# Kernel optimization log

Hardware: AMD Instinct MI355X
Metric: run time of the kernel (lower is better)

Reference implementation:

```python
import jax, jax.numpy as jnp
import numpy as np

B, T, DIN, DOUT = 64, 128, 32, 64
HE, HD, K = 512, 1024, 12
NPH, NPL = 512, 64
# per-sample decoder parameter layout: Whh, bh, Wih, C, D
_PSI_SHAPES = [(HD, HD), (HD,), (DIN, HD), (HD, DOUT), (DIN, DOUT - DIN)]
_PSI_SIZES = [int(np.prod(s)) for s in _PSI_SHAPES]
_PSI_OFF = np.cumsum([0] + _PSI_SIZES)
NPSI = int(_PSI_OFF[-1])


def _xavier(key, shape):
    fan_in, fan_out = shape[-2], shape[-1]
    lim = np.sqrt(6.0 / (fan_in + fan_out))
    return jax.random.uniform(key, shape, jnp.float32, -lim, lim)


def setup_inputs() -> dict:
    key = jax.random.key(0)
    ks = jax.random.split(key, 16)
    gru_bias = jnp.concatenate([jnp.zeros(HD), jnp.ones(HD)])  # z-gate bias init to 1
    return {
        'inputs': jax.random.normal(ks[0], (B, T, DIN), jnp.float32),
        'outputs': jax.random.normal(ks[1], (B, T, DOUT), jnp.float32),
        'eps': jax.random.normal(ks[2], (B, K), jnp.float32),
        'state': jnp.zeros((B, HD), jnp.float32),
        'enc_Wih': _xavier(ks[3], (3 * HE, DOUT)),
        'enc_Whh': _xavier(ks[4], (3 * HE, HE)),
        'enc_bih': jnp.zeros(3 * HE, jnp.float32),
        'enc_bhh': jnp.zeros(3 * HE, jnp.float32),
        'to_mu': _xavier(ks[5], (HE, K)),
        'to_lsigma': _xavier(ks[6], (HE, K)),
        'to_lsigma_bias': -0.5 * jnp.ones(K, jnp.float32),
        'psi_W1': _xavier(ks[7], (K, NPH)),
        'psi_b1': jnp.zeros(NPH, jnp.float32),
        'psi_W2': _xavier(ks[8], (NPH, NPL)),
        'psi_b2': jnp.zeros(NPL, jnp.float32),
        'psi_W3': _xavier(ks[9], (NPL, NPSI)) * 0.05,
        'psi_b3': jnp.zeros(NPSI, jnp.float32),
        'gru_Wih': _xavier(ks[10], (DIN, 2 * HD)),
        'gru_Whh': _xavier(ks[11], (HD, 2 * HD)),
        'gru_bias': gru_bias,
    }


def _forward(inputs, outputs, eps, state, enc_Wih, enc_Whh, enc_bih, enc_bhh,
             to_mu, to_lsigma, to_lsigma_bias, psi_W1, psi_b1, psi_W2, psi_b2,
             psi_W3, psi_b3, gru_Wih, gru_Whh, gru_bias):
    # ---- encoder: shared GRUCell over time (torch GRUCell semantics) ----
    def enc_step(h, x):
        gi = x @ enc_Wih.T + enc_bih          # [B,3HE]
        gh = h @ enc_Whh.T + enc_bhh
        ir, iz, inn = jnp.split(gi, 3, axis=-1)
        hr, hz, hn = jnp.split(gh, 3, axis=-1)
        r = jax.nn.sigmoid(ir + hr)
        z = jax.nn.sigmoid(iz + hz)
        n = jnp.tanh(inn + r * hn)
        return (1.0 - z) * n + z * h, None
    h0 = jnp.zeros((outputs.shape[0], HE), outputs.dtype)
    h_enc, _ = jax.lax.scan(enc_step, h0, jnp.swapaxes(outputs, 0, 1))

    mu = h_enc @ to_mu
    logstd = h_enc @ to_lsigma + to_lsigma_bias
    z_lat = mu + eps * jnp.exp(logstd)

    # ---- hypernetwork: decode per-sample GRU params ----
    psi = (jnp.tanh(z_lat @ psi_W1 + psi_b1) @ psi_W2 + psi_b2) @ psi_W3 + psi_b3  # [B,NPSI]
    parts = [psi[:, _PSI_OFF[i]:_PSI_OFF[i + 1]].reshape((-1,) + _PSI_SHAPES[i])
             for i in range(5)]
    Whh_b, bh_b, Wih_b, C_b, D_b = parts

    # ---- per-sample partial GRU over time (batched via einsum) ----
    def dec_step(h, x):
        gx = x @ gru_Wih                       # [B,2HD] shared gates
        gh = h @ gru_Whh
        r = jax.nn.sigmoid(gx[:, :HD] + gh[:, :HD] + gru_bias[:HD])
        zt = jax.nn.sigmoid(gx[:, HD:] + gh[:, HD:] + gru_bias[HD:])
        eta = jnp.tanh(jnp.einsum('bi,bih->bh', x, Wih_b)
                       + r * jnp.einsum('bh,bhg->bg', h, Whh_b) + bh_b)
        h_new = zt * h + (1.0 - zt) * eta
        return h_new, h_new
    _, dec = jax.lax.scan(dec_step, state, jnp.swapaxes(inputs, 0, 1))
    dec = jnp.swapaxes(dec, 0, 1)              # [B,T,HD]

    # residual_output with HUMAN_SIZE > input_dim: concat(raw inputs, inputs@D)
    resid = jnp.concatenate([inputs, jnp.einsum('bti,bio->bto', inputs, D_b)], axis=-1)
    yhats = jnp.einsum('bth,bho->bto', dec, C_b) + resid
    states = jax.lax.stop_gradient(dec[:, -1, :])
    return yhats, mu, logstd, states


def reference(inputs, outputs, eps, state, enc_Wih, enc_Whh, enc_bih, enc_bhh,
              to_mu, to_lsigma, to_lsigma_bias, psi_W1, psi_b1, psi_W2, psi_b2,
              psi_W3, psi_b3, gru_Wih, gru_Whh, gru_bias):
    return _forward(inputs, outputs, eps, state, enc_Wih, enc_Whh, enc_bih, enc_bhh,
                    to_mu, to_lsigma, to_lsigma_bias, psi_W1, psi_b1, psi_W2, psi_b2,
                    psi_W3, psi_b3, gru_Wih, gru_Whh, gru_bias)
```

## Files before the change

kernel.cpp:

```cpp
#include <hip/hip_runtime.h>
#include <stdint.h>

#define B_ 64
#define T_ 128
#define DIN_ 32
#define DOUT_ 64
#define HE_ 512
#define HD_ 1024
#define NPSI_ 1148928
#define PPS_ 100352

typedef short bf16x8 __attribute__((ext_vector_type(8)));
typedef float f32x4 __attribute__((ext_vector_type(4)));
typedef int   i32x4 __attribute__((ext_vector_type(4)));

__device__ __forceinline__ unsigned short f2b(float f){
  unsigned u = __float_as_uint(f);
  u += 0x7fffu + ((u>>16)&1u);
  return (unsigned short)(u>>16);
}
__device__ __forceinline__ float b2f(unsigned short s){
  return __uint_as_float(((unsigned)s)<<16);
}
__device__ __forceinline__ float sigm_(float x){
  float e = __expf(-x);
  return 1.f/(1.f+e);
}
__device__ __forceinline__ float tanh_(float x){
  float e = __expf(2.f*x);
  return 1.f - 2.f/(e+1.f);
}
__device__ __forceinline__ void glds16(const void* g, void* l) {
  __builtin_amdgcn_global_load_lds(
      (const __attribute__((address_space(1))) unsigned int*)g,
      (__attribute__((address_space(3))) unsigned int*)l, 16, 0, 0);
}

__global__ __launch_bounds__(512) void k_prep(
    const float* __restrict__ enc_Whh, const float* __restrict__ enc_Wih,
    const float* __restrict__ gru_Whh, const float* __restrict__ state,
    unsigned short* __restrict__ encW_f, unsigned short* __restrict__ encI_f,
    signed char* __restrict__ gru_q, float* __restrict__ scales_g,
    unsigned short* __restrict__ h_dec)
{
  __shared__ unsigned gmax_s;
  __shared__ __align__(16) signed char gq[512];
  int blk = blockIdx.x, tid = threadIdx.x;
  if (blk < 1536) {
    int nt = blk >> 4, kt = blk & 15;
    int c = tid >> 5, k = tid & 31;
    float v = enc_Whh[(size_t)(nt*16 + c)*HE_ + kt*32 + k];
    int l = c + ((k>>3)<<4), jj = k & 7;
    encW_f[(size_t)(nt*16 + kt)*512 + l*8 + jj] = f2b(v);
  } else if (blk < 1728) {
    int f = blk - 1536; int nt = f >> 1, kt = f & 1;
    int c = tid >> 5, k = tid & 31;
    float v = enc_Wih[(size_t)(nt*16 + c)*DOUT_ + kt*32 + k];
    int l = c + ((k>>3)<<4), jj = k & 7;
    encI_f[(size_t)(nt*2 + kt)*512 + l*8 + jj] = f2b(v);
  } else if (blk < 5824) {
    int f = blk - 1728; int nt = f >> 5, kt = f & 31;
    int k = tid >> 4, c = tid & 15;
    float v = gru_Whh[(size_t)(kt*32 + k)*2048 + nt*16 + c];
    int l = c + ((k>>3)<<4), jj = k & 7;
    if (tid == 0) gmax_s = 0;
    __syncthreads();
    float av = fabsf(v);
    #pragma unroll
    for (int d = 1; d < 64; d <<= 1) av = fmaxf(av, __shfl_xor(av, d));
    if ((tid & 63) == 0) atomicMax(&gmax_s, __float_as_uint(av));
    __syncthreads();
    float m = __uint_as_float(gmax_s);
    float inv = (m > 0.f) ? (127.f/m) : 0.f;
    gq[l*8 + jj] = (signed char)(int)rintf(v*inv);
    __syncthreads();
    if (tid < 32)
      *(i32x4*)(gru_q + (size_t)(nt*32 + kt)*512 + tid*16) = *(const i32x4*)(&gq[tid*16]);
    if (tid == 0) scales_g[nt*32 + kt] = m;
  } else {
    int b = blk - 5824;
    h_dec[(size_t)b*HD_ + tid]       = f2b(state[(size_t)b*HD_ + tid]);
    h_dec[(size_t)b*HD_ + 512 + tid] = f2b(state[(size_t)b*HD_ + 512 + tid]);
  }
}

__global__ __launch_bounds__(128) void k_encoder(
    const float* __restrict__ outputs, const float* __restrict__ bih, const float* __restrict__ bhh,
    const unsigned short* __restrict__ encW_f, const unsigned short* __restrict__ encI_f,
    unsigned short* __restrict__ h_buf, float* __restrict__ h_enc, unsigned int* __restrict__ bar)
{
  __shared__ __align__(16) unsigned short h_bf[16*520];
  __shared__ __align__(16) unsigned short xa[16*72];
  __shared__ float part[64*16];
  int tid = threadIdx.x, wv = tid >> 6, lane = tid & 63;
  int g = blockIdx.x >> 5, bg = blockIdx.x & 31;
  int c0 = bg*16, gs = g*8;
  for (int i = tid; i < 16*520; i += 128) h_bf[i] = 0;
  for (int i = tid; i < 16*72; i += 128) xa[i] = 0;
  int cl = c0 + (lane & 15);
  float br_b = bih[cl] + bhh[cl];
  float bz_b = bih[512+cl] + bhh[512+cl];
  float bin_b = bih[1024+cl];
  float bhn_b = bhh[1024+cl];
  float hreg[4] = {0.f,0.f,0.f,0.f};
  int row = (lane>>4)<<2;
  int nt_r = bg, nt_z = 32+bg, nt_n = 64+bg;
  __syncthreads();
  for (int t = 0; t < 128; ++t) {
    int rb = t & 1;
    if (t > 0) {
      if (tid == 0) {
        while (__hip_atomic_load(&bar[(g<<7)+(t-1)], __ATOMIC_ACQUIRE, __HIP_MEMORY_SCOPE_AGENT) < 32u)
          __builtin_amdgcn_s_sleep(2);
      }
      __syncthreads();
    }
    {
      const unsigned short* src = h_buf + (size_t)rb*B_*HE_ + (size_t)gs*HE_;
      #pragma unroll
      for (int j = 0; j < 4; ++j) {
        int chunk = j*128 + tid;
        bf16x8 v = *(const bf16x8*)(src + chunk*8);
        int s = chunk >> 6, col = (chunk & 63) * 8;
        *(bf16x8*)(&h_bf[s*520 + col]) = v;
      }
      #pragma unroll
      for (int j = 0; j < 4; ++j) {
        int e = j*128 + tid;
        int s = e >> 6, d = e & 63;
        xa[s*72 + d] = f2b(outputs[((size_t)(gs+s)*T_ + t)*DOUT_ + d]);
      }
    }
    __syncthreads();
    f32x4 accr = {0,0,0,0}, accz = {0,0,0,0}, accn = {0,0,0,0}, accgi = {0,0,0,0};
    {
      bf16x8 a = *(const bf16x8*)(&xa[(lane&15)*72 + wv*32 + ((lane>>4)<<3)]);
      bf16x8 b0 = *(const bf16x8*)(encI_f + (size_t)(nt_r*2+wv)*512 + lane*8);
      bf16x8 b1 = *(const bf16x8*)(encI_f + (size_t)(nt_z*2+wv)*512 + lane*8);
      bf16x8 b2 = *(const bf16x8*)(encI_f + (size_t)(nt_n*2+wv)*512 + lane*8);
      accr  = __builtin_amdgcn_mfma_f32_16x16x32_bf16(a, b0, accr, 0,0,0);
      accz  = __builtin_amdgcn_mfma_f32_16x16x32_bf16(a, b1, accz, 0,0,0);
      accgi = __builtin_amdgcn_mfma_f32_16x16x32_bf16(a, b2, accgi, 0,0,0);
    }
    #pragma unroll
    for (int kk = 0; kk < 8; ++kk) {
      int kt = wv*8 + kk;
      bf16x8 a = *(const bf16x8*)(&h_bf[(lane&15)*520 + kt*32 + ((lane>>4)<<3)]);
      bf16x8 b0 = *(const bf16x8*)(encW_f + (size_t)(nt_r*16+kt)*512 + lane*8);
      bf16x8 b1 = *(const bf16x8*)(encW_f + (size_t)(nt_z*16+kt)*512 + lane*8);
      bf16x8 b2 = *(const bf16x8*)(encW_f + (size_t)(nt_n*16+kt)*512 + lane*8);
      accr = __builtin_amdgcn_mfma_f32_16x16x32_bf16(a, b0, accr, 0,0,0);
      accz = __builtin_amdgcn_mfma_f32_16x16x32_bf16(a, b1, accz, 0,0,0);
      accn = __builtin_amdgcn_mfma_f32_16x16x32_bf16(a, b2, accn, 0,0,0);
    }
    if (wv == 1) {
      #pragma unroll
      for (int i = 0; i < 4; ++i) {
        part[lane*16 + i]      = accr[i];
        part[lane*16 + 4 + i]  = accz[i];
        part[lane*16 + 8 + i]  = accn[i];
        part[lane*16 + 12 + i] = accgi[i];
      }
    }
    __syncthreads();
    if (wv == 0 && row < 8) {
      unsigned short* dst = h_buf + (size_t)(rb^1)*B_*HE_;
      #pragma unroll
      for (int i = 0; i < 4; ++i) {
        int s = row + i;
        float ar  = accr[i]  + part[lane*16 + i];
        float az  = accz[i]  + part[lane*16 + 4 + i];
        float an  = accn[i]  + part[lane*16 + 8 + i];
        float agi = accgi[i] + part[lane*16 + 12 + i];
        float r = sigm_(ar + br_b);
        float z = sigm_(az + bz_b);
        float n = tanh_(agi + bin_b + r*(an + bhn_b));
        float hn = (1.f - z)*n + z*hreg[i];
        hreg[i] = hn;
        dst[(size_t)(gs+s)*HE_ + cl] = f2b(hn);
        if (t == 127) h_enc[(size_t)(gs+s)*HE_ + cl] = hn;
      }
    }
    __syncthreads();
    if (tid == 0)
      __hip_atomic_fetch_add(&bar[(g<<7)+t], 1u, __ATOMIC_ACQ_REL, __HIP_MEMORY_SCOPE_AGENT);
  }
}

__global__ __launch_bounds__(64) void k_latent(
    const float* __restrict__ h_enc, const float* __restrict__ to_mu,
    const float* __restrict__ to_ls, const float* __restrict__ ls_bias,
    const float* __restrict__ eps, float* __restrict__ out_mu,
    float* __restrict__ out_ls, float* __restrict__ z_lat)
{
  __shared__ float hb[512];
  int b = blockIdx.x, tid = threadIdx.x;
  #pragma unroll
  for (int j = 0; j < 8; ++j) hb[j*64 + tid] = h_enc[(size_t)b*HE_ + j*64 + tid];
  __syncthreads();
  if (tid < 12) {
    float m = 0.f, s = 0.f;
    #pragma unroll 8
    for (int k = 0; k < 512; ++k) {
      float h = hb[k];
      m += h * to_mu[k*12 + tid];
      s += h * to_ls[k*12 + tid];
    }
    s += ls_bias[tid];
    out_mu[b*12 + tid] = m;
    out_ls[b*12 + tid] = s;
    z_lat[b*12 + tid] = m + eps[b*12 + tid] * __expf(s);
  }
}

__global__ __launch_bounds__(512) void k_hidden(
    const float* __restrict__ z_lat, const float* __restrict__ W1, const float* __restrict__ b1,
    const float* __restrict__ W2, const float* __restrict__ b2, float* __restrict__ hidden_T)
{
  __shared__ float zl[12];
  __shared__ float a[512];
  int b = blockIdx.x, tid = threadIdx.x;
  if (tid < 12) zl[tid] = z_lat[b*12 + tid];
  __syncthreads();
  float acc = b1[tid];
  #pragma unroll
  for (int k = 0; k < 12; ++k) acc += zl[k] * W1[k*512 + tid];
  a[tid] = tanh_(acc);
  __syncthreads();
  if (tid < 64) {
    float h = b2[tid];
    #pragma unroll 8
    for (int j = 0; j < 512; ++j) h += a[j] * W2[j*64 + tid];
    hidden_T[tid*64 + b] = h;
  }
}

__global__ __launch_bounds__(1024) void k_psi(
    const float* __restrict__ hidden_T, const float* __restrict__ W3, const float* __restrict__ b3,
    signed char* __restrict__ whh_q, float* __restrict__ scales, float* __restrict__ params)
{
  __shared__ float hid[64*64];
  __shared__ unsigned lmax[32];
  __shared__ __align__(16) signed char qtile[32*1024];
  int tid = threadIdx.x, blk = blockIdx.x;
  if (tid < 32) lmax[tid] = 0;
  #pragma unroll
  for (int j = 0; j < 4; ++j) hid[j*1024 + tid] = hidden_T[j*1024 + tid];
  __syncthreads();
  bool is_whh = blk < 2048;
  if (is_whh) {
    int kt = blk >> 6, cp = (blk >> 1) & 31, bh = blk & 1;
    int i_loc = tid >> 5, c_loc = tid & 31;
    size_t j = (size_t)(kt*32 + i_loc)*1024 + cp*32 + c_loc;
    float bv = b3[j];
    float acc[32];
    #pragma unroll
    for (int b = 0; b < 32; ++b) acc[b] = bv;
    for (int k = 0; k < 64; ++k) {
      float wv = W3[(size_t)k*NPSI_ + j];
      #pragma unroll
      for (int bq = 0; bq < 8; ++bq) {
        f32x4 h4 = *(const f32x4*)(&hid[k*64 + bh*32 + bq*4]);
        acc[bq*4+0] += wv * h4[0];
        acc[bq*4+1] += wv * h4[1];
        acc[bq*4+2] += wv * h4[2];
        acc[bq*4+3] += wv * h4[3];
      }
    }
    #pragma unroll
    for (int b = 0; b < 32; ++b) {
      float av = fabsf(acc[b]);
      #pragma unroll
      for (int d = 1; d < 64; d <<= 1) av = fmaxf(av, __shfl_xor(av, d));
      if ((tid & 63) == 0) atomicMax(&lmax[b], __float_as_uint(av));
    }
    __syncthreads();
    int l = (c_loc & 15) + (((i_loc>>3)&3)<<4);
    int jj = i_loc & 7;
    int base_lds = ((c_loc>>4)<<9) + l*8 + jj;
    #pragma unroll
    for (int b = 0; b < 32; ++b) {
      float m = __uint_as_float(lmax[b]);
      float inv = (m > 0.f) ? (127.f/m) : 0.f;
      qtile[b*1024 + base_lds] = (signed char)(int)rintf(acc[b]*inv);
    }
    __syncthreads();
    #pragma unroll
    for (int it = 0; it < 2; ++it) {
      int qid = it*1024 + tid;
      int b = qid >> 6, c64 = qid & 63;
      i32x4 v = *(const i32x4*)(&qtile[b*1024 + c64*16]);
      size_t goff = (size_t)(bh*32 + b)*1048576
                  + (size_t)((2*cp + (c64>>5))*32 + kt)*512 + (c64&31)*16;
      *(i32x4*)(whh_q + goff) = v;
    }
    if (tid < 32)
      scales[(size_t)(bh*32 + tid)*1024 + kt*32 + cp] = __uint_as_float(lmax[tid]);
  } else {
    size_t j = (size_t)1048576 + (size_t)(blk - 2048)*1024 + tid;
    float bv = b3[j];
    float acc[64];
    #pragma unroll
    for (int b = 0; b < 64; ++b) acc[b] = bv;
    for (int k = 0; k < 64; ++k) {
      float wv = W3[(size_t)k*NPSI_ + j];
      #pragma unroll
      for (int bq = 0; bq < 16; ++bq) {
        f32x4 h4 = *(const f32x4*)(&hid[k*64 + bq*4]);
        acc[bq*4+0] += wv * h4[0];
        acc[bq*4+1] += wv * h4[1];
        acc[bq*4+2] += wv * h4[2];
        acc[bq*4+3] += wv * h4[3];
      }
    }
    size_t off = j - 1048576;
    #pragma unroll
    for (int b = 0; b < 64; ++b)
      params[(size_t)b*PPS_ + off] = acc[b];
  }
}

__global__ __launch_bounds__(512, 2) void k_decoder(
    const float* __restrict__ inputs, const float* __restrict__ gru_Wih,
    const float* __restrict__ gru_bias,
    const signed char* __restrict__ whh_q, const float* __restrict__ scales,
    const signed char* __restrict__ gru_q, const float* __restrict__ scales_g,
    const float* __restrict__ params,
    unsigned short* __restrict__ h_buf, float* __restrict__ dec,
    float* __restrict__ out_states, unsigned int* __restrict__ bar)
{
  __shared__ __align__(16) unsigned short h_bf[8*1048];
  __shared__ __align__(16) signed char h_q8[8*1040];
  __shared__ __align__(16) char stg[8][2][5120];
  __shared__ unsigned short wih_lds[8192];
  __shared__ unsigned short gwih_lds[2048];
  __shared__ float x_lds[256];
  __shared__ float gh_lds[1024];
  __shared__ float mv_lds[256];
  __shared__ float sc_lds[256];
  __shared__ float sgr_lds[128];
  int tid = threadIdx.x;
  int g = blockIdx.x >> 5, bg = blockIdx.x & 31;
  int c0 = bg*32, gs = g*8;
  int w = tid >> 6, lane = tid & 63;
  int s_t = (tid >> 5) & 7, c_t = tid & 31;
  int sg_t = gs + s_t, cg_t = c0 + c_t;
  float bh_r = 0.f, br_b = 0.f, bz_b = 0.f;
  if (tid < 256) {
    bh_r = params[(size_t)sg_t*PPS_ + cg_t];
    br_b = gru_bias[cg_t];
    bz_b = gru_bias[1024 + cg_t];
  }
  for (int idx = tid; idx < 2048; idx += 512) {
    int i = idx >> 6, gc = idx & 63;
    gwih_lds[idx] = f2b(gru_Wih[i*2048 + (gc>>5)*1024 + c0 + (gc&31)]);
  }
  for (int idx = tid; idx < 8192; idx += 512) {
    int s = idx >> 10, r = idx & 1023;
    wih_lds[idx] = f2b(params[(size_t)(gs+s)*PPS_ + 1024 + (r>>5)*1024 + c0 + (r&31)]);
  }
  if (lane < 32)
    sc_lds[w*32 + lane] = scales[(size_t)(gs+w)*1024 + lane*32 + bg] * (1.f/16129.f);
  int j_t = w >> 1;
  int nt_j = (j_t < 2) ? (2*bg + j_t) : (64 + 2*bg + (j_t - 2));
  if (lane < 16)
    sgr_lds[w*16 + lane] = scales_g[nt_j*32 + (w&1)*16 + lane] * (1.f/16129.f);
  const char* af0c = (const char*)whh_q + (size_t)((gs+w)*64 + 2*bg)*16384 + lane*16;
  const char* af1c = af0c + 16384;
  const char* gfc = (const char*)gru_q + ((size_t)nt_j*32 + (w&1)*16)*512 + lane*16;
  int ho_l = (lane>>4)<<3;
  int ghk0 = (w&1)*16;
  char* bufA = &stg[w][0][0];
  char* bufB = &stg[w][1][0];

  auto ISSUE = [&](char* bufp, int cc) {
    const char* a0 = af0c + (size_t)cc*2048;
    const char* a1 = af1c + (size_t)cc*2048;
    glds16(a0,        bufp);        glds16(a0 + 1024, bufp + 1024);
    glds16(a1,        bufp + 2048); glds16(a1 + 1024, bufp + 3072);
    glds16(gfc + (size_t)cc*1024, bufp + 4096);
  };
  f32x4 aghf, facc0, facc1;
  auto HALF = [&](char* bufp, int c) {
    asm volatile("s_waitcnt vmcnt(5)" ::: "memory");
    long a00 = *(const long*)(bufp + 0*512 + lane*8);
    long a01 = *(const long*)(bufp + 1*512 + lane*8);
    long a02 = *(const long*)(bufp + 2*512 + lane*8);
    long a03 = *(const long*)(bufp + 3*512 + lane*8);
    long a10 = *(const long*)(bufp + 2048 + 0*512 + lane*8);
    long a11 = *(const long*)(bufp + 2048 + 1*512 + lane*8);
    long a12 = *(const long*)(bufp + 2048 + 2*512 + lane*8);
    long a13 = *(const long*)(bufp + 2048 + 3*512 + lane*8);
    long qg0 = *(const long*)(bufp + 4096 + lane*8);
    long qg1 = *(const long*)(bufp + 4608 + lane*8);
    long hq0 = *(const long*)(h_q8 + w*1040 + (4*c+0)*32 + ho_l);
    long hq1 = *(const long*)(h_q8 + w*1040 + (4*c+1)*32 + ho_l);
    long hq2 = *(const long*)(h_q8 + w*1040 + (4*c+2)*32 + ho_l);
    long hq3 = *(const long*)(h_q8 + w*1040 + (4*c+3)*32 + ho_l);
    long haq0 = *(const long*)(h_q8 + (lane&15)*1040 + (ghk0 + 2*c)*32 + ho_l);
    long haq1 = *(const long*)(h_q8 + (lane&15)*1040 + (ghk0 + 2*c+1)*32 + ho_l);
    float s0 = sc_lds[w*32 + 4*c + 0];
    float s1 = sc_lds[w*32 + 4*c + 1];
    float s2 = sc_lds[w*32 + 4*c + 2];
    float s3 = sc_lds[w*32 + 4*c + 3];
    float g0 = sgr_lds[w*16 + 2*c], g1 = sgr_lds[w*16 + 2*c + 1];
    asm volatile("s_waitcnt lgkmcnt(0)" ::: "memory");
    __builtin_amdgcn_sched_barrier(0);
    ISSUE(bufp, (c + 2) & 7);
    i32x4 z4 = {0,0,0,0};
    i32x4 q;
    q = __builtin_amdgcn_mfma_i32_16x16x32_i8(a00, hq0, z4, 0,0,0);
    #pragma unroll
    for (int e = 0; e < 4; ++e) facc0[e] += (float)q[e]*s0;
    q = __builtin_amdgcn_mfma_i32_16x16x32_i8(a01, hq1, z4, 0,0,0);
    #pragma unroll
    for (int e = 0; e < 4; ++e) facc0[e] += (float)q[e]*s1;
    q = __builtin_amdgcn_mfma_i32_16x16x32_i8(a02, hq2, z4, 0,0,0);
    #pragma unroll
    for (int e = 0; e < 4; ++e) facc0[e] += (float)q[e]*s2;
    q = __builtin_amdgcn_mfma_i32_16x16x32_i8(a03, hq3, z4, 0,0,0);
    #pragma unroll
    for (int e = 0; e < 4; ++e) facc0[e] += (float)q[e]*s3;
    q = __builtin_amdgcn_mfma_i32_16x16x32_i8(a10, hq0, z4, 0,0,0);
    #pragma unroll
    for (int e = 0; e < 4; ++e) facc1[e] += (float)q[e]*s0;
    q = __builtin_amdgcn_mfma_i32_16x16x32_i8(a11, hq1, z4, 0,0,0);
    #pragma unroll
    for (int e = 0; e < 4; ++e) facc1[e] += (float)q[e]*s1;
    q = __builtin_amdgcn_mfma_i32_16x16x32_i8(a12, hq2, z4, 0,0,0);
    #pragma unroll
    for (int e = 0; e < 4; ++e) facc1[e] += (float)q[e]*s2;
    q = __builtin_amdgcn_mfma_i32_16x16x32_i8(a13, hq3, z4, 0,0,0);
    #pragma unroll
    for (int e = 0; e < 4; ++e) facc1[e] += (float)q[e]*s3;
    q = __builtin_amdgcn_mfma_i32_16x16x32_i8(haq0, qg0, z4, 0,0,0);
    #pragma unroll
    for (int e = 0; e < 4; ++e) aghf[e] += (float)q[e]*g0;
    q = __builtin_amdgcn_mfma_i32_16x16x32_i8(haq1, qg1, z4, 0,0,0);
    #pragma unroll
    for (int e = 0; e < 4; ++e) aghf[e] += (float)q[e]*g1;
  };

  __syncthreads();
  ISSUE(bufA, 0); ISSUE(bufB, 1);
  for (int t = 0; t < 128; ++t) {
    int rb = t & 1;
    if (t > 0 && tid == 0) {
      while (__hip_atomic_load(&bar[(g<<7)+(t-1)], __ATOMIC_ACQUIRE, __HIP_MEMORY_SCOPE_AGENT) < 32u)
        __builtin_amdgcn_s_sleep(1);
    }
    __builtin_amdgcn_s_barrier();
    {
      const char* hs = (const char*)(h_buf + (size_t)rb*B_*HD_ + (size_t)(gs + w)*HD_) + lane*16;
      glds16(hs,        &h_bf[w*1048]);
      glds16(hs + 1024, &h_bf[w*1048 + 512]);
    }
    if (tid < 256) x_lds[tid] = inputs[((size_t)sg_t*T_ + t)*DIN_ + c_t];
    asm volatile("s_waitcnt vmcnt(0)" ::: "memory");
    {
      i32x4 pk;
      #pragma unroll
      for (int hh = 0; hh < 2; ++hh) {
        bf16x8 hv = *(const bf16x8*)(&h_bf[w*1048 + lane*16 + hh*8]);
        int lo = 0, hi2 = 0;
        #pragma unroll
        for (int e = 0; e < 4; ++e) {
          int q = (int)rintf(b2f((unsigned short)hv[e]) * 127.f);
          lo |= (q & 255) << (8*e);
        }
        #pragma unroll
        for (int e = 0; e < 4; ++e) {
          int q = (int)rintf(b2f((unsigned short)hv[4+e]) * 127.f);
          hi2 |= (q & 255) << (8*e);
        }
        pk[2*hh] = lo; pk[2*hh+1] = hi2;
      }
      *(i32x4*)(h_q8 + w*1040 + lane*16) = pk;
    }
    asm volatile("s_waitcnt lgkmcnt(0)" ::: "memory");
    __builtin_amdgcn_s_barrier();
    aghf = (f32x4){0,0,0,0}; facc0 = (f32x4){0,0,0,0}; facc1 = (f32x4){0,0,0,0};
    #pragma unroll 1
    for (int i2 = 0; i2 < 4; ++i2) {
      HALF(bufA, 2*i2);
      HALF(bufB, 2*i2 + 1);
    }
    if (lane < 32) {
      #pragma unroll
      for (int i = 0; i < 4; ++i)
        gh_lds[w*128 + ((lane>>4)*4 + i)*16 + (lane&15)] = aghf[i];
    }
    if ((lane & 15) == 0) {
      int cb = (lane>>4)*4;
      #pragma unroll
      for (int i = 0; i < 4; ++i) {
        mv_lds[w*32 + cb + i]      = facc0[i];
        mv_lds[w*32 + 16 + cb + i] = facc1[i];
      }
    }
    asm volatile("s_waitcnt lgkmcnt(0)" ::: "memory");
    __builtin_amdgcn_s_barrier();
    if (tid < 256) {
      int jr = c_t >> 4, cl16 = c_t & 15;
      float ghr = gh_lds[(2*jr)*128   + s_t*16 + cl16] + gh_lds[(2*jr+1)*128 + s_t*16 + cl16];
      float ghz = gh_lds[(4+2*jr)*128 + s_t*16 + cl16] + gh_lds[(5+2*jr)*128 + s_t*16 + cl16];
      float gxr = 0.f, gxz = 0.f, ex = 0.f;
      #pragma unroll 8
      for (int i = 0; i < 32; ++i) {
        float xv = x_lds[s_t*32 + i];
        gxr += xv * b2f(gwih_lds[i*64 + c_t]);
        gxz += xv * b2f(gwih_lds[i*64 + 32 + c_t]);
        ex  += xv * b2f(wih_lds[s_t*1024 + i*32 + c_t]);
      }
      float r = sigm_(gxr + ghr + br_b);
      float z = sigm_(gxz + ghz + bz_b);
      float eta = tanh_(ex + bh_r + r * mv_lds[s_t*32 + c_t]);
      float ho_ = b2f(h_bf[s_t*1048 + c0 + c_t]);
      float hn = z*ho_ + (1.f - z)*eta;
      dec[((size_t)sg_t*T_ + t)*HD_ + cg_t] = hn;
      h_buf[(size_t)(rb^1)*B_*HD_ + (size_t)sg_t*HD_ + cg_t] = f2b(hn);
      if (t == 127) out_states[(size_t)sg_t*HD_ + cg_t] = hn;
    }
    asm volatile("s_waitcnt vmcnt(0)" ::: "memory");
    __builtin_amdgcn_s_barrier();
    if (t < 127 && tid == 0)
      __hip_atomic_fetch_add(&bar[(g<<7)+t], 1u, __ATOMIC_ACQ_REL, __HIP_MEMORY_SCOPE_AGENT);
  }
}

__global__ __launch_bounds__(256) void k_yhats(
    const float* __restrict__ dec, const float* __restrict__ inputs,
    const float* __restrict__ params, float* __restrict__ out_y)
{
  __shared__ __align__(16) float dsm[8*1024];
  __shared__ float xr[8*32];
  int blk = blockIdx.x, tid = threadIdx.x;
  int b = blk >> 4, t8 = (blk & 15) * 8;
  const float* prm = params + (size_t)b*PPS_;
  const float* C = prm + 33792;
  const float* D = prm + 99328;
  #pragma unroll
  for (int j = 0; j < 8; ++j) {
    int ch = j*256 + tid;
    *(f32x4*)(&dsm[ch*4]) = *(const f32x4*)(dec + ((size_t)b*T_ + t8)*HD_ + ch*4);
  }
  {
    int tl = tid >> 5, i = tid & 31;
    xr[tl*32 + i] = inputs[((size_t)b*T_ + t8 + tl)*DIN_ + i];
    xr[(tl+4)*32 + i] = inputs[((size_t)b*T_ + t8 + tl + 4)*DIN_ + i];
  }
  __syncthreads();
  int o = tid & 63;
  int tl0 = (tid >> 6) * 2;
  float a0 = 0.f, a1 = 0.f;
  #pragma unroll 4
  for (int h = 0; h < 1024; ++h) {
    float cv = C[h*64 + o];
    a0 += dsm[tl0*1024 + h] * cv;
    a1 += dsm[(tl0+1)*1024 + h] * cv;
  }
  float r0, r1;
  if (o < 32) {
    r0 = xr[tl0*32 + o];
    r1 = xr[(tl0+1)*32 + o];
  } else {
    r0 = 0.f; r1 = 0.f;
    #pragma unroll 8
    for (int i = 0; i < 32; ++i) {
      float dv = D[i*32 + (o-32)];
      r0 += xr[tl0*32 + i] * dv;
      r1 += xr[(tl0+1)*32 + i] * dv;
    }
  }
  out_y[((size_t)b*T_ + t8 + tl0)*DOUT_ + o]     = a0 + r0;
  out_y[((size_t)b*T_ + t8 + tl0 + 1)*DOUT_ + o] = a1 + r1;
}

extern "C" void kernel_launch(void* const* d_in, const int* in_sizes, int n_in,
                              void* d_out, int out_size, void* d_ws, size_t ws_size,
                              hipStream_t stream)
{
  const float* inputs  = (const float*)d_in[0];
  const float* outputs = (const float*)d_in[1];
  const float* eps     = (const float*)d_in[2];
  const float* state   = (const float*)d_in[3];
  const float* enc_Wih = (const float*)d_in[4];
  const float* enc_Whh = (const float*)d_in[5];
  const float* enc_bih = (const float*)d_in[6];
  const float* enc_bhh = (const float*)d_in[7];
  const float* to_mu   = (const float*)d_in[8];
  const float* to_ls   = (const float*)d_in[9];
  const float* to_lsb  = (const float*)d_in[10];
  const float* psi_W1  = (const float*)d_in[11];
  const float* psi_b1  = (const float*)d_in[12];
  const float* psi_W2  = (const float*)d_in[13];
  const float* psi_b2  = (const float*)d_in[14];
  const float* psi_W3  = (const float*)d_in[15];
  const float* psi_b3  = (const float*)d_in[16];
  const float* gru_Wih = (const float*)d_in[17];
  const float* gru_Whh = (const float*)d_in[18];
  const float* gru_bias= (const float*)d_in[19];
  float* out    = (float*)d_out;
  float* out_y  = out;
  float* out_mu = out + 524288;
  float* out_ls = out + 525056;
  float* out_st = out + 525824;

  if (ws_size < 130000000) return;
  char* ws = (char*)d_ws;
  size_t off = 0;
  auto alloc = [&](size_t bytes)->char*{ char* p = ws + off; off += (bytes + 255) & ~(size_t)255; return p; };
  signed char* whh_q      = (signed char*)alloc(67108864);
  float* scales           = (float*)alloc(262144);
  unsigned short* encW_f  = (unsigned short*)alloc(1572864);
  unsigned short* encI_f  = (unsigned short*)alloc(196608);
  signed char* gru_q      = (signed char*)alloc(2097152);
  float* scales_g         = (float*)alloc(16384);
  float* params           = (float*)alloc(25690112);
  float* h_enc            = (float*)alloc(131072);
  float* z_lat            = (float*)alloc(3072);
  float* hidden_T         = (float*)alloc(16384);
  unsigned short* h_buf_e = (unsigned short*)alloc(131072);
  unsigned short* h_buf_d = (unsigned short*)alloc(262144);
  float* dec              = (float*)alloc(33554432);
  unsigned int* bar_e     = (unsigned int*)alloc(8192);
  unsigned int* bar_d     = (unsigned int*)alloc(8192);

  hipMemsetAsync(bar_e, 0, 8192, stream);
  hipMemsetAsync(bar_d, 0, 8192, stream);
  hipMemsetAsync(h_buf_e, 0, 131072, stream);

  k_prep<<<5888, 512, 0, stream>>>(enc_Whh, enc_Wih, gru_Whh, state, encW_f, encI_f, gru_q, scales_g, h_buf_d);
  k_encoder<<<256, 128, 0, stream>>>(outputs, enc_bih, enc_bhh, encW_f, encI_f, h_buf_e, h_enc, bar_e);
  k_latent<<<64, 64, 0, stream>>>(h_enc, to_mu, to_ls, to_lsb, eps, out_mu, out_ls, z_lat);
  k_hidden<<<64, 512, 0, stream>>>(z_lat, psi_W1, psi_b1, psi_W2, psi_b2, hidden_T);
  k_psi<<<2146, 1024, 0, stream>>>(hidden_T, psi_W3, psi_b3, whh_q, scales, params);
  k_decoder<<<256, 512, 0, stream>>>(inputs, gru_Wih, gru_bias, whh_q, scales, gru_q, scales_g, params, h_buf_d, dec, out_st, bar_d);
  k_yhats<<<1024, 256, 0, stream>>>(dec, inputs, params, out_y);
}
```

Before: 4.329 ms.

## Use per-wave grid barrier in decoder, spread epilogue over waves, fuse latent kernels

The decoder's per-step cross-block barrier changes from one thread per block waiting plus a workgroup s_barrier to every wave spinning on the global counter and each wave signalling arrival itself, so the counter target goes from 32 to 256. The gate epilogue is remapped so each of the 8 waves handles one sample with 32 active lanes instead of using only the first 4 waves, and the trailing workgroup barrier is dropped. The latent and hidden kernels are fused into one launch, removing the z_lat round trip. This adds more atomic traffic and spinning waves per step, and relies on each wave's own writes being ordered before its atomic increment.

```diff
diff --git a/kernel.cpp b/kernel.cpp
--- a/kernel.cpp
+++ b/kernel.cpp
@@ -187,16 +187,20 @@
   }
 }
 
-__global__ __launch_bounds__(64) void k_latent(
+__global__ __launch_bounds__(512) void k_lathid(
     const float* __restrict__ h_enc, const float* __restrict__ to_mu,
     const float* __restrict__ to_ls, const float* __restrict__ ls_bias,
     const float* __restrict__ eps, float* __restrict__ out_mu,
-    float* __restrict__ out_ls, float* __restrict__ z_lat)
+    float* __restrict__ out_ls,
+    const float* __restrict__ W1, const float* __restrict__ b1,
+    const float* __restrict__ W2, const float* __restrict__ b2,
+    float* __restrict__ hidden_T)
 {
   __shared__ float hb[512];
+  __shared__ float zl[12];
+  __shared__ float a[512];
   int b = blockIdx.x, tid = threadIdx.x;
-  #pragma unroll
-  for (int j = 0; j < 8; ++j) hb[j*64 + tid] = h_enc[(size_t)b*HE_ + j*64 + tid];
+  hb[tid] = h_enc[(size_t)b*HE_ + tid];
   __syncthreads();
   if (tid < 12) {
     float m = 0.f, s = 0.f;
@@ -209,18 +213,8 @@
     s += ls_bias[tid];
     out_mu[b*12 + tid] = m;
     out_ls[b*12 + tid] = s;
-    z_lat[b*12 + tid] = m + eps[b*12 + tid] * __expf(s);
-  }
-}
-
-__global__ __launch_bounds__(512) void k_hidden(
-    const float* __restrict__ z_lat, const float* __restrict__ W1, const float* __restrict__ b1,
-    const float* __restrict__ W2, const float* __restrict__ b2, float* __restrict__ hidden_T)
-{
-  __shared__ float zl[12];
-  __shared__ float a[512];
-  int b = blockIdx.x, tid = threadIdx.x;
-  if (tid < 12) zl[tid] = z_lat[b*12 + tid];
+    zl[tid] = m + eps[b*12 + tid] * __expf(s);
+  }
   __syncthreads();
   float acc = b1[tid];
   #pragma unroll
@@ -344,12 +338,12 @@
   int c0 = bg*32, gs = g*8;
   int w = tid >> 6, lane = tid & 63;
   int s_t = (tid >> 5) & 7, c_t = tid & 31;
-  int sg_t = gs + s_t, cg_t = c0 + c_t;
+  int sg_t = gs + s_t;
   float bh_r = 0.f, br_b = 0.f, bz_b = 0.f;
-  if (tid < 256) {
-    bh_r = params[(size_t)sg_t*PPS_ + cg_t];
-    br_b = gru_bias[cg_t];
-    bz_b = gru_bias[1024 + cg_t];
+  if (lane < 32) {
+    bh_r = params[(size_t)(gs+w)*PPS_ + c0 + lane];
+    br_b = gru_bias[c0 + lane];
+    bz_b = gru_bias[1024 + c0 + lane];
   }
   for (int idx = tid; idx < 2048; idx += 512) {
     int i = idx >> 6, gc = idx & 63;
@@ -445,11 +439,10 @@
   ISSUE(bufA, 0); ISSUE(bufB, 1);
   for (int t = 0; t < 128; ++t) {
     int rb = t & 1;
-    if (t > 0 && tid == 0) {
-      while (__hip_atomic_load(&bar[(g<<7)+(t-1)], __ATOMIC_ACQUIRE, __HIP_MEMORY_SCOPE_AGENT) < 32u)
-        __builtin_amdgcn_s_sleep(1);
-    }
-    __builtin_amdgcn_s_barrier();
+    if (t > 0) {
+      while (__hip_atomic_load(&bar[(g<<7)+(t-1)], __ATOMIC_ACQUIRE, __HIP_MEMORY_SCOPE_AGENT) < 256u)
+        __builtin_amdgcn_s_sleep(2);
+    }
     {
       const char* hs = (const char*)(h_buf + (size_t)rb*B_*HD_ + (size_t)(gs + w)*HD_) + lane*16;
       glds16(hs,        &h_bf[w*1048]);
@@ -500,30 +493,29 @@
     }
     asm volatile("s_waitcnt lgkmcnt(0)" ::: "memory");
     __builtin_amdgcn_s_barrier();
-    if (tid < 256) {
-      int jr = c_t >> 4, cl16 = c_t & 15;
-      float ghr = gh_lds[(2*jr)*128   + s_t*16 + cl16] + gh_lds[(2*jr+1)*128 + s_t*16 + cl16];
-      float ghz = gh_lds[(4+2*jr)*128 + s_t*16 + cl16] + gh_lds[(5+2*jr)*128 + s_t*16 + cl16];
+    if (lane < 32) {
+      int jr = lane >> 4, cl16 = lane & 15;
+      float ghr = gh_lds[(2*jr)*128   + w*16 + cl16] + gh_lds[(2*jr+1)*128 + w*16 + cl16];
+      float ghz = gh_lds[(4+2*jr)*128 + w*16 + cl16] + gh_lds[(5+2*jr)*128 + w*16 + cl16];
       float gxr = 0.f, gxz = 0.f, ex = 0.f;
       #pragma unroll 8
       for (int i = 0; i < 32; ++i) {
-        float xv = x_lds[s_t*32 + i];
-        gxr += xv * b2f(gwih_lds[i*64 + c_t]);
-        gxz += xv * b2f(gwih_lds[i*64 + 32 + c_t]);
-        ex  += xv * b2f(wih_lds[s_t*1024 + i*32 + c_t]);
+        float xv = x_lds[w*32 + i];
+        gxr += xv * b2f(gwih_lds[i*64 + lane]);
+        gxz += xv * b2f(gwih_lds[i*64 + 32 + lane]);
+        ex  += xv * b2f(wih_lds[w*1024 + i*32 + lane]);
       }
       float r = sigm_(gxr + ghr + br_b);
       float z = sigm_(gxz + ghz + bz_b);
-      float eta = tanh_(ex + bh_r + r * mv_lds[s_t*32 + c_t]);
-      float ho_ = b2f(h_bf[s_t*1048 + c0 + c_t]);
+      float eta = tanh_(ex + bh_r + r * mv_lds[w*32 + lane]);
+      float ho_ = b2f(h_bf[w*1048 + c0 + lane]);
       float hn = z*ho_ + (1.f - z)*eta;
-      dec[((size_t)sg_t*T_ + t)*HD_ + cg_t] = hn;
-      h_buf[(size_t)(rb^1)*B_*HD_ + (size_t)sg_t*HD_ + cg_t] = f2b(hn);
-      if (t == 127) out_states[(size_t)sg_t*HD_ + cg_t] = hn;
+      dec[((size_t)(gs+w)*T_ + t)*HD_ + c0 + lane] = hn;
+      h_buf[(size_t)(rb^1)*B_*HD_ + (size_t)(gs+w)*HD_ + c0 + lane] = f2b(hn);
+      if (t == 127) out_states[(size_t)(gs+w)*HD_ + c0 + lane] = hn;
     }
     asm volatile("s_waitcnt vmcnt(0)" ::: "memory");
-    __builtin_amdgcn_s_barrier();
-    if (t < 127 && tid == 0)
+    if (t < 127 && lane == 0)
       __hip_atomic_fetch_add(&bar[(g<<7)+t], 1u, __ATOMIC_ACQ_REL, __HIP_MEMORY_SCOPE_AGENT);
   }
 }
@@ -618,7 +610,6 @@
   float* scales_g         = (float*)alloc(16384);
   float* params           = (float*)alloc(25690112);
   float* h_enc            = (float*)alloc(131072);
-  float* z_lat            = (float*)alloc(3072);
   float* hidden_T         = (float*)alloc(16384);
   unsigned short* h_buf_e = (unsigned short*)alloc(131072);
   unsigned short* h_buf_d = (unsigned short*)alloc(262144);
@@ -632,8 +623,8 @@
 
   k_prep<<<5888, 512, 0, stream>>>(enc_Whh, enc_Wih, gru_Whh, state, encW_f, encI_f, gru_q, scales_g, h_buf_d);
   k_encoder<<<256, 128, 0, stream>>>(outputs, enc_bih, enc_bhh, encW_f, encI_f, h_buf_e, h_enc, bar_e);
-  k_latent<<<64, 64, 0, stream>>>(h_enc, to_mu, to_ls, to_lsb, eps, out_mu, out_ls, z_lat);
-  k_hidden<<<64, 512, 0, stream>>>(z_lat, psi_W1, psi_b1, psi_W2, psi_b2, hidden_T);
+  k_lathid<<<64, 512, 0, stream>>>(h_enc, to_mu, to_ls, to_lsb, eps, out_mu, out_ls,
+                                   psi_W1, psi_b1, psi_W2, psi_b2, hidden_T);
   k_psi<<<2146, 1024, 0, stream>>>(hidden_T, psi_W3, psi_b3, whh_q, scales, params);
   k_decoder<<<256, 512, 0, stream>>>(inputs, gru_Wih, gru_bias, whh_q, scales, gru_q, scales_g, params, h_buf_d, dec, out_st, bar_d);
   k_yhats<<<1024, 256, 0, stream>>>(dec, inputs, params, out_y);
```

New measurement: 11.52 ms. 166% more time.
